# Performance work log

Hardware: AMD Instinct MI355X
Metric: run time of the kernel (lower is better)

## Reference

```python
import jax, jax.numpy as jnp
import numpy as np

_INV_SQRT2 = np.float32(0.7071067811865476)


def _dwt_last(u):
    """Single-level Haar DWT along the last axis (pywt 'haar' convention).
    cA[i] = (u[2i]+u[2i+1])/sqrt(2), cD[i] = (u[2i]-u[2i+1])/sqrt(2)."""
    e = u[..., 0::2]
    o = u[..., 1::2]
    return (e + o) * _INV_SQRT2, (e - o) * _INV_SQRT2


def _dwt2(x):
    """Single-level 2D Haar DWT over the last two axes, matching pywt.dwt2.
    Returns (cA, cH, cV, cD) = ('aa', 'da', 'ad', 'dd') where the first
    letter is the filter applied along axis -2 and the second along axis -1."""
    a1, d1 = _dwt_last(x)                      # filter along axis -1
    a1t, d1t = a1.swapaxes(-1, -2), d1.swapaxes(-1, -2)
    aa, da = _dwt_last(a1t)                    # filter along axis -2
    ad, dd = _dwt_last(d1t)
    return (aa.swapaxes(-1, -2), da.swapaxes(-1, -2),
            ad.swapaxes(-1, -2), dd.swapaxes(-1, -2))


def setup_inputs() -> dict:
    key = jax.random.key(0)
    B, C, H, W = 32, 3, 512, 512
    x = jax.random.normal(key, (B, C, H, W), dtype=jnp.float32)
    return {"x": x}


def reference(x):
    # pywt.wavedec2(x, 'haar', level=2) -> [cA2, (cH2,cV2,cD2), (cH1,cV1,cD1)]
    a1, h1, v1, d1 = _dwt2(x)    # level 1: [B,C,H/2,W/2]
    a2, h2, v2, d2 = _dwt2(a1)   # level 2: [B,C,H/4,W/4]
    return (a2, h2, v2, d2, h1, v1, d1)
```

## Files before the change

kernel.cpp:

```cpp
#include <hip/hip_runtime.h>


#define KINV 0.7071067811865476f

typedef float v4f __attribute__((ext_vector_type(4)));
typedef float v2f __attribute__((ext_vector_type(2)));

#define STRIPE_ROWS 16
#define LDS_FLOATS (STRIPE_ROWS * 512)

__global__ __launch_bounds__(256) void haar2_fused_kernel(
    const float* __restrict__ x, float* __restrict__ out, int nimg)
{
    __shared__ float lds[LDS_FLOATS];

    const int tid  = threadIdx.x;
    const int lane = tid & 63;
    const int w    = tid >> 6;
    const int blk    = blockIdx.x;
    const int stripe = blk & 31;
    const int img    = blk >> 5;

    const size_t n2 = (size_t)nimg * 128 * 128;
    const size_t n1 = (size_t)nimg * 256 * 256;
    float* a2o = out;
    float* h2o = out + n2;
    float* v2o = out + 2 * n2;
    float* d2o = out + 3 * n2;
    float* h1o = out + 4 * n2;
    float* v1o = h1o + n1;
    float* d1o = h1o + 2 * n1;

    const size_t stripe_base =
        (size_t)img * (512 * 512) + (size_t)stripe * (STRIPE_ROWS * 512);

    {
        const float* gsrc = x + stripe_base + (size_t)(w * 2048) + (size_t)(lane * 4);
        float* ldst = &lds[w * 2048];
        #pragma unroll
        for (int j = 0; j < 8; ++j) {
            __builtin_amdgcn_global_load_lds(
                (const __attribute__((address_space(1))) void*)(gsrc + j * 256),
                (__attribute__((address_space(3))) void*)(ldst + j * 256),
                16, 0, 0);
        }
    }
    asm volatile("s_waitcnt vmcnt(0)" ::: "memory");
    __builtin_amdgcn_sched_barrier(0);

    const int cx = lane;
    v4f L[4], R[4];
    #pragma unroll
    for (int r = 0; r < 4; ++r) {
        const float* p = &lds[(w * 4 + r) * 512 + cx * 8];
        L[r] = *reinterpret_cast<const v4f*>(p);
        R[r] = *reinterpret_cast<const v4f*>(p + 4);
    }

    float aaL[2][2], daL[2][2], adL[2][2], ddL[2][2];
    float aaR[2][2], daR[2][2], adR[2][2], ddR[2][2];
    #pragma unroll
    for (int i = 0; i < 2; ++i) {
        {
            const v4f top = L[2 * i], bot = L[2 * i + 1];
            const float sA0 = (top.x + top.y) * KINV, dA0 = (top.x - top.y) * KINV;
            const float sB0 = (bot.x + bot.y) * KINV, dB0 = (bot.x - bot.y) * KINV;
            aaL[i][0] = (sA0 + sB0) * KINV; daL[i][0] = (sA0 - sB0) * KINV;
            adL[i][0] = (dA0 + dB0) * KINV; ddL[i][0] = (dA0 - dB0) * KINV;
            const float sA1 = (top.z + top.w) * KINV, dA1 = (top.z - top.w) * KINV;
            const float sB1 = (bot.z + bot.w) * KINV, dB1 = (bot.z - bot.w) * KINV;
            aaL[i][1] = (sA1 + sB1) * KINV; daL[i][1] = (sA1 - sB1) * KINV;
            adL[i][1] = (dA1 + dB1) * KINV; ddL[i][1] = (dA1 - dB1) * KINV;
        }
        {
            const v4f top = R[2 * i], bot = R[2 * i + 1];
            const float sA0 = (top.x + top.y) * KINV, dA0 = (top.x - top.y) * KINV;
            const float sB0 = (bot.x + bot.y) * KINV, dB0 = (bot.x - bot.y) * KINV;
            aaR[i][0] = (sA0 + sB0) * KINV; daR[i][0] = (sA0 - sB0) * KINV;
            adR[i][0] = (dA0 + dB0) * KINV; ddR[i][0] = (dA0 - dB0) * KINV;
            const float sA1 = (top.z + top.w) * KINV, dA1 = (top.z - top.w) * KINV;
            const float sB1 = (bot.z + bot.w) * KINV, dB1 = (bot.z - bot.w) * KINV;
            aaR[i][1] = (sA1 + sB1) * KINV; daR[i][1] = (sA1 - sB1) * KINV;
            adR[i][1] = (dA1 + dB1) * KINV; ddR[i][1] = (dA1 - dB1) * KINV;
        }
    }

    const size_t img1 = (size_t)img * 256 * 256;
    const int l1row = stripe * 8 + w * 2;
    #pragma unroll
    for (int i = 0; i < 2; ++i) {
        const size_t off = img1 + (size_t)(l1row + i) * 256 + (size_t)cx * 4;
        __builtin_nontemporal_store((v4f){daL[i][0], daL[i][1], daR[i][0], daR[i][1]},
                                    reinterpret_cast<v4f*>(h1o + off));
        __builtin_nontemporal_store((v4f){adL[i][0], adL[i][1], adR[i][0], adR[i][1]},
                                    reinterpret_cast<v4f*>(v1o + off));
        __builtin_nontemporal_store((v4f){ddL[i][0], ddL[i][1], ddR[i][0], ddR[i][1]},
                                    reinterpret_cast<v4f*>(d1o + off));
    }

    const float s0L = (aaL[0][0] + aaL[0][1]) * KINV;
    const float d0L = (aaL[0][0] - aaL[0][1]) * KINV;
    const float s1L = (aaL[1][0] + aaL[1][1]) * KINV;
    const float d1L = (aaL[1][0] - aaL[1][1]) * KINV;
    const float s0R = (aaR[0][0] + aaR[0][1]) * KINV;
    const float d0R = (aaR[0][0] - aaR[0][1]) * KINV;
    const float s1R = (aaR[1][0] + aaR[1][1]) * KINV;
    const float d1R = (aaR[1][0] - aaR[1][1]) * KINV;

    const size_t off2 = (size_t)img * (128 * 128)
                      + (size_t)(stripe * 4 + w) * 128 + (size_t)cx * 2;
    __builtin_nontemporal_store((v2f){(s0L + s1L) * KINV, (s0R + s1R) * KINV},
                                reinterpret_cast<v2f*>(a2o + off2));
    __builtin_nontemporal_store((v2f){(s0L - s1L) * KINV, (s0R - s1R) * KINV},
                                reinterpret_cast<v2f*>(h2o + off2));
    __builtin_nontemporal_store((v2f){(d0L + d1L) * KINV, (d0R + d1R) * KINV},
                                reinterpret_cast<v2f*>(v2o + off2));
    __builtin_nontemporal_store((v2f){(d0L - d1L) * KINV, (d0R - d1R) * KINV},
                                reinterpret_cast<v2f*>(d2o + off2));
}

extern "C" void kernel_launch(void* const* d_in, const int* in_sizes, int n_in,
                              void* d_out, int out_size, void* d_ws, size_t ws_size,
                              hipStream_t stream) {
    const float* x = (const float*)d_in[0];
    float* out = (float*)d_out;
    const int nimg = in_sizes[0] / (512 * 512);
    const int grid = nimg * 32;
    const int block = 256;
    haar2_fused_kernel<<<grid, block, 0, stream>>>(x, out, nimg);
}
```

Measured before the change: 176.5 us.

## Replace LDS staging with direct global loads and XCD-aware block remap

Removes the 64KB LDS stripe staging via global_load_lds and instead has each thread load its 4x8 input patch directly from global memory with 16-byte vector loads. The grid is reindexed at one thread per 4x8 patch with block IDs remapped so consecutive logical blocks land on the same XCD, and launch bounds request 4 waves per EU. Dropping LDS is meant to raise occupancy and cut the full-wait stall. The trade-off is that each lane now reads two adjacent 16-byte chunks 32 bytes apart, which is less coalesced per instruction than the old contiguous lane pattern.

```diff
diff --git a/kernel.cpp b/kernel.cpp
--- a/kernel.cpp
+++ b/kernel.cpp
@@ -6,20 +6,23 @@
 typedef float v4f __attribute__((ext_vector_type(4)));
 typedef float v2f __attribute__((ext_vector_type(2)));
 
-#define STRIPE_ROWS 16
-#define LDS_FLOATS (STRIPE_ROWS * 512)
+#define NXCD 8
 
-__global__ __launch_bounds__(256) void haar2_fused_kernel(
+__global__ __launch_bounds__(256, 4) void haar2_fused_kernel(
     const float* __restrict__ x, float* __restrict__ out, int nimg)
 {
-    __shared__ float lds[LDS_FLOATS];
+    const int nwg = (int)gridDim.x;
+    const int cpx = nwg / NXCD;
+    const int bid = (int)blockIdx.x;
+    const int lbid = (bid % NXCD) * cpx + (bid / NXCD);
 
-    const int tid  = threadIdx.x;
-    const int lane = tid & 63;
-    const int w    = tid >> 6;
-    const int blk    = blockIdx.x;
-    const int stripe = blk & 31;
-    const int img    = blk >> 5;
+    const int tid = lbid * (int)blockDim.x + (int)threadIdx.x;
+    const int cx  = tid & 63;
+    const int r2  = (tid >> 6) & 127;
+    const int img = tid >> 13;
+
+    const int row0 = r2 * 4;
+    const int col0 = cx * 8;
 
     const size_t n2 = (size_t)nimg * 128 * 128;
     const size_t n1 = (size_t)nimg * 256 * 256;
@@ -31,30 +34,12 @@
     float* v1o = h1o + n1;
     float* d1o = h1o + 2 * n1;
 
-    const size_t stripe_base =
-        (size_t)img * (512 * 512) + (size_t)stripe * (STRIPE_ROWS * 512);
-
-    {
-        const float* gsrc = x + stripe_base + (size_t)(w * 2048) + (size_t)(lane * 4);
-        float* ldst = &lds[w * 2048];
-        #pragma unroll
-        for (int j = 0; j < 8; ++j) {
-            __builtin_amdgcn_global_load_lds(
-                (const __attribute__((address_space(1))) void*)(gsrc + j * 256),
-                (__attribute__((address_space(3))) void*)(ldst + j * 256),
-                16, 0, 0);
-        }
-    }
-    asm volatile("s_waitcnt vmcnt(0)" ::: "memory");
-    __builtin_amdgcn_sched_barrier(0);
-
-    const int cx = lane;
-    v4f L[4], R[4];
+    const size_t in_base = (size_t)img * (512 * 512) + (size_t)row0 * 512 + col0;
+    v4f bA[4], bB[4];
     #pragma unroll
-    for (int r = 0; r < 4; ++r) {
-        const float* p = &lds[(w * 4 + r) * 512 + cx * 8];
-        L[r] = *reinterpret_cast<const v4f*>(p);
-        R[r] = *reinterpret_cast<const v4f*>(p + 4);
+    for (int k = 0; k < 4; ++k) {
+        bA[k] = *reinterpret_cast<const v4f*>(x + in_base + (size_t)k * 512);
+        bB[k] = *reinterpret_cast<const v4f*>(x + in_base + (size_t)k * 512 + 4);
     }
 
     float aaL[2][2], daL[2][2], adL[2][2], ddL[2][2];
@@ -62,7 +47,7 @@
     #pragma unroll
     for (int i = 0; i < 2; ++i) {
         {
-            const v4f top = L[2 * i], bot = L[2 * i + 1];
+            const v4f top = bA[2 * i], bot = bA[2 * i + 1];
             const float sA0 = (top.x + top.y) * KINV, dA0 = (top.x - top.y) * KINV;
             const float sB0 = (bot.x + bot.y) * KINV, dB0 = (bot.x - bot.y) * KINV;
             aaL[i][0] = (sA0 + sB0) * KINV; daL[i][0] = (sA0 - sB0) * KINV;
@@ -73,7 +58,7 @@
             adL[i][1] = (dA1 + dB1) * KINV; ddL[i][1] = (dA1 - dB1) * KINV;
         }
         {
-            const v4f top = R[2 * i], bot = R[2 * i + 1];
+            const v4f top = bB[2 * i], bot = bB[2 * i + 1];
             const float sA0 = (top.x + top.y) * KINV, dA0 = (top.x - top.y) * KINV;
             const float sB0 = (bot.x + bot.y) * KINV, dB0 = (bot.x - bot.y) * KINV;
             aaR[i][0] = (sA0 + sB0) * KINV; daR[i][0] = (sA0 - sB0) * KINV;
@@ -86,10 +71,9 @@
     }
 
     const size_t img1 = (size_t)img * 256 * 256;
-    const int l1row = stripe * 8 + w * 2;
     #pragma unroll
     for (int i = 0; i < 2; ++i) {
-        const size_t off = img1 + (size_t)(l1row + i) * 256 + (size_t)cx * 4;
+        const size_t off = img1 + (size_t)(2 * r2 + i) * 256 + (size_t)cx * 4;
         __builtin_nontemporal_store((v4f){daL[i][0], daL[i][1], daR[i][0], daR[i][1]},
                                     reinterpret_cast<v4f*>(h1o + off));
         __builtin_nontemporal_store((v4f){adL[i][0], adL[i][1], adR[i][0], adR[i][1]},
@@ -107,8 +91,7 @@
     const float s1R = (aaR[1][0] + aaR[1][1]) * KINV;
     const float d1R = (aaR[1][0] - aaR[1][1]) * KINV;
 
-    const size_t off2 = (size_t)img * (128 * 128)
-                      + (size_t)(stripe * 4 + w) * 128 + (size_t)cx * 2;
+    const size_t off2 = (size_t)img * 128 * 128 + (size_t)r2 * 128 + 2 * cx;
     __builtin_nontemporal_store((v2f){(s0L + s1L) * KINV, (s0R + s1R) * KINV},
                                 reinterpret_cast<v2f*>(a2o + off2));
     __builtin_nontemporal_store((v2f){(s0L - s1L) * KINV, (s0R - s1R) * KINV},
@@ -125,7 +108,8 @@
     const float* x = (const float*)d_in[0];
     float* out = (float*)d_out;
     const int nimg = in_sizes[0] / (512 * 512);
-    const int grid = nimg * 32;
+    const int total_threads = nimg * 128 * 64;
     const int block = 256;
+    const int grid = total_threads / block;
     haar2_fused_kernel<<<grid, block, 0, stream>>>(x, out, nimg);
 }
```

Measured after the change: 177.4 us. Within noise of the previous version (+0.6%).
